# Optimization experiments

Measured on AMD Instinct MI355X. Metric: run time of the kernel, lower is better.

Reference implementation:

```python
import jax, jax.numpy as jnp
import numpy as np

D = 128
N1, N2, N3, N4 = 100000, 200000, 300000, 400000


def setup_inputs() -> dict:
    key = jax.random.key(0)
    cnt = [0]

    def nrm(shape, scale=0.05):
        cnt[0] += 1
        return jax.random.normal(jax.random.fold_in(key, cnt[0]), shape, dtype=jnp.float32) * scale

    def rint(shape, hi):
        cnt[0] += 1
        return jax.random.randint(jax.random.fold_in(key, cnt[0]), shape, 0, hi)

    inp = {}
    inp["h"] = nrm((N1, D), 1.0)
    inp["idx2"] = rint((N2, 2), N1)
    inp["idx3"] = rint((N3, 3), N1)
    inp["idx4"] = rint((N4, 4), N1)
    # sequential_%L MLPs: Linear(L*D -> D) + relu, Linear(D->D)+relu, Linear(D->D)+relu
    for L in (1, 2, 3, 4):
        din = D * L
        inp["s%d_W0" % L] = nrm((din, D))
        inp["s%d_b0" % L] = nrm((D,))
        inp["s%d_W1" % L] = nrm((D, D))
        inp["s%d_b1" % L] = nrm((D,))
        inp["s%d_W2" % L] = nrm((D, D))
        inp["s%d_b2" % L] = nrm((D,))
    # per-feature output heads Linear(D -> 1)
    for f in ("sigma", "epsilon", "q"):
        inp["h1_%s_W" % f] = nrm((D, 1))
        inp["h1_%s_b" % f] = nrm((1,))
    for L in (2, 3, 4):
        for f in ("k", "eq"):
            inp["h%d_%s_W" % (L, f)] = nrm((D, 1))
            inp["h%d_%s_b" % (L, f)] = nrm((1,))
    return inp


def _mlp(x, W0, b0, W1, b1, W2, b2):
    x = jax.nn.relu(x @ W0 + b0)
    x = jax.nn.relu(x @ W1 + b1)
    return jax.nn.relu(x @ W2 + b2)


def _level(h, idx, p):
    # copy_u + mean with exactly one n1 neighbor per relationship slot == gather
    g = jnp.take(h, idx, axis=0)              # [N, K, D]
    N, K, Dd = g.shape
    xf = g.reshape(N, K * Dd)                 # concat h0..h_{K-1}
    xb = g[:, ::-1, :].reshape(N, K * Dd)     # concat reversed
    return _mlp(xf, *p) + _mlp(xb, *p)        # pool = torch.add


def reference(h, idx2, idx3, idx4,
              s1_W0, s1_b0, s1_W1, s1_b1, s1_W2, s1_b2,
              s2_W0, s2_b0, s2_W1, s2_b1, s2_W2, s2_b2,
              s3_W0, s3_b0, s3_W1, s3_b1, s3_W2, s3_b2,
              s4_W0, s4_b0, s4_W1, s4_b1, s4_W2, s4_b2,
              h1_sigma_W, h1_sigma_b, h1_epsilon_W, h1_epsilon_b, h1_q_W, h1_q_b,
              h2_k_W, h2_k_b, h2_eq_W, h2_eq_b,
              h3_k_W, h3_k_b, h3_eq_W, h3_eq_b,
              h4_k_W, h4_k_b, h4_eq_W, h4_eq_b):
    y1 = _mlp(h, s1_W0, s1_b0, s1_W1, s1_b1, s1_W2, s1_b2)
    sigma = y1 @ h1_sigma_W + h1_sigma_b
    epsilon = y1 @ h1_epsilon_W + h1_epsilon_b
    q = y1 @ h1_q_W + h1_q_b
    y2 = _level(h, idx2, (s2_W0, s2_b0, s2_W1, s2_b1, s2_W2, s2_b2))
    k2 = y2 @ h2_k_W + h2_k_b
    eq2 = y2 @ h2_eq_W + h2_eq_b
    y3 = _level(h, idx3, (s3_W0, s3_b0, s3_W1, s3_b1, s3_W2, s3_b2))
    k3 = y3 @ h3_k_W + h3_k_b
    eq3 = y3 @ h3_eq_W + h3_eq_b
    y4 = _level(h, idx4, (s4_W0, s4_b0, s4_W1, s4_b1, s4_W2, s4_b2))
    k4 = y4 @ h4_k_W + h4_k_b
    eq4 = y4 @ h4_eq_W + h4_eq_b
    return (sigma, epsilon, q, k2, eq2, k3, eq3, k4, eq4)
```

## Files before the change

### kernel.cpp

```cpp
#include <hip/hip_runtime.h>

typedef __attribute__((ext_vector_type(8))) _Float16 half8;
typedef __attribute__((ext_vector_type(4))) float f32x4;

#define N1_ 100000
#define N2_ 200000
#define N3_ 300000
#define N4_ 400000

typedef __attribute__((address_space(1))) const void gconst_t;
typedef __attribute__((address_space(3))) void lds_t;

__device__ __forceinline__ unsigned short f2h_bits(float x) {
  union { _Float16 h; unsigned short u; } cv;
  cv.h = (_Float16)x;
  return cv.u;
}

__device__ __forceinline__ f32x4 mfma16(half8 a, half8 b, f32x4 c) {
  return __builtin_amdgcn_mfma_f32_16x16x32_f16(a, b, c, 0, 0, 0);
}

__global__ void cvt_h_kernel(const float* __restrict__ h,
                             unsigned short* __restrict__ hf, int n4) {
  int i = blockIdx.x * blockDim.x + threadIdx.x;
  if (i >= n4) return;
  float4 v = reinterpret_cast<const float4*>(h)[i];
  ushort4 o;
  o.x = f2h_bits(v.x); o.y = f2h_bits(v.y);
  o.z = f2h_bits(v.z); o.w = f2h_bits(v.w);
  reinterpret_cast<ushort4*>(hf)[i] = o;
}

struct PackInfo {
  const float* W[12];
  int kt_base[13];
  int out_off[12];
};

__global__ void pack_w_kernel(PackInfo info, unsigned short* __restrict__ pw) {
  int b = blockIdx.x;
  int lane = threadIdx.x;
  int m = 0;
  while (m < 11 && b >= info.kt_base[m + 1]) ++m;
  int kt = b - info.kt_base[m];
  const float* W = info.W[m];
  int lr = lane & 15, kb = lane >> 4;
  unsigned short* outp = pw + info.out_off[m] + (size_t)kt * 4096 + lane * 8;
  #pragma unroll
  for (int nt = 0; nt < 8; ++nt) {
    #pragma unroll
    for (int j = 0; j < 8; ++j) {
      int krow = kt * 32 + kb * 8 + j;
      int col = nt * 16 + lr;
      outp[nt * 512 + j] = f2h_bits(W[(size_t)krow * 128 + col]);
    }
  }
}

template <int K, int NHEAD>
__global__ __launch_bounds__(256, 3) void level_kernel(
    const unsigned short* __restrict__ hf,
    const int* __restrict__ idx,
    const unsigned short* __restrict__ pw,
    const float* __restrict__ b0, const float* __restrict__ b1,
    const float* __restrict__ b2,
    const float* __restrict__ hw0, const float* __restrict__ hb0,
    float* __restrict__ out0,
    const float* __restrict__ hw1, const float* __restrict__ hb1,
    float* __restrict__ out1,
    const float* __restrict__ hw2, const float* __restrict__ hb2,
    float* __restrict__ out2,
    int N) {
  constexpr int NDIR = (K > 1) ? 2 : 1;
  constexpr int KT0 = 4 * K;

  __shared__ __align__(16) unsigned short bstage[2][4096];
  __shared__ __align__(16) unsigned short act[4][NDIR][2048];

  const int lane = threadIdx.x & 63;
  const int wid = threadIdx.x >> 6;
  const int lrow = lane & 15;
  const int kb = lane >> 4;

  int tile = blockIdx.x * 4 + wid;
  const int maxtile = N / 16 - 1;
  const bool writer = (tile <= maxtile);
  if (!writer) tile = maxtile;
  const int row = tile * 16 + lrow;

  int src[K];
  #pragma unroll
  for (int s = 0; s < K; ++s) src[s] = (K == 1) ? row : idx[(size_t)row * K + s];

  auto stage = [&](int buf, const unsigned short* slab) {
    #pragma unroll
    for (int c = 0; c < 2; ++c) {
      const unsigned short* g = slab + (wid * 2 + c) * 512 + lane * 8;
      unsigned short* l = &bstage[buf][(wid * 2 + c) * 512];
      __builtin_amdgcn_global_load_lds((gconst_t*)g, (lds_t*)l, 16, 0, 0);
    }
  };

  int cur = 0;
  auto run_layer = [&](const unsigned short* w, int nkt, auto&& getAf,
                       auto&& getAb, f32x4* accF, f32x4* accB) {
    stage(cur, w);
    __syncthreads();
    for (int kt = 0; kt < nkt; ++kt) {
      if (kt + 1 < nkt) stage(cur ^ 1, w + (size_t)(kt + 1) * 4096);
      half8 af = getAf(kt);
      half8 ab;
      if constexpr (NDIR == 2) ab = getAb(kt);
      #pragma unroll
      for (int nt = 0; nt < 8; ++nt) {
        half8 bq = *reinterpret_cast<const half8*>(&bstage[cur][nt * 512 + lane * 8]);
        accF[nt] = mfma16(af, bq, accF[nt]);
        if constexpr (NDIR == 2) accB[nt] = mfma16(ab, bq, accB[nt]);
      }
      __syncthreads();
      cur ^= 1;
    }
  };

  auto A0f = [&](int kt) {
    int seg = kt >> 2, sub = kt & 3;
    return *reinterpret_cast<const half8*>(hf + (size_t)src[seg] * 128 + sub * 32 + kb * 8);
  };
  auto A0b = [&](int kt) {
    int seg = K - 1 - (kt >> 2), sub = kt & 3;
    return *reinterpret_cast<const half8*>(hf + (size_t)src[seg] * 128 + sub * 32 + kb * 8);
  };
  auto actRead = [&](int dir, int kt) -> half8 {
    unsigned off = (unsigned)(lrow * 256 + (kt * 32 + kb * 8) * 2) ^ ((unsigned)(lrow & 7) << 4);
    return *reinterpret_cast<const half8*>(
        reinterpret_cast<const unsigned char*>(&act[wid][dir][0]) + off);
  };
  auto actA0 = [&](int kt) { return actRead(0, kt); };
  auto actA1 = [&](int kt) { return actRead(NDIR == 2 ? 1 : 0, kt); };

  auto store_act = [&](const f32x4* acc, const float* bias, int dir) {
    unsigned char* base = reinterpret_cast<unsigned char*>(&act[wid][dir][0]);
    #pragma unroll
    for (int nt = 0; nt < 8; ++nt) {
      float bv = bias[nt * 16 + lrow];
      #pragma unroll
      for (int r = 0; r < 4; ++r) {
        float v = fmaxf(acc[nt][r] + bv, 0.f);
        int trow = 4 * kb + r;
        unsigned off = (unsigned)(trow * 256 + (nt * 16 + lrow) * 2) ^ ((unsigned)(trow & 7) << 4);
        *reinterpret_cast<unsigned short*>(base + off) = f2h_bits(v);
      }
    }
  };

  f32x4 aF[8], aB[8];
  auto zero_acc = [&](f32x4* a) {
    #pragma unroll
    for (int nt = 0; nt < 8; ++nt) a[nt] = f32x4{0.f, 0.f, 0.f, 0.f};
  };

  zero_acc(aF); zero_acc(aB);
  run_layer(pw, KT0, A0f, A0b, aF, aB);
  store_act(aF, b0, 0);
  if constexpr (NDIR == 2) store_act(aB, b0, 1);

  zero_acc(aF); zero_acc(aB);
  run_layer(pw + (size_t)KT0 * 4096, 4, actA0, actA1, aF, aB);
  store_act(aF, b1, 0);
  if constexpr (NDIR == 2) store_act(aB, b1, 1);

  zero_acc(aF); zero_acc(aB);
  run_layer(pw + (size_t)KT0 * 4096 + 16384, 4, actA0, actA1, aF, aB);

  f32x4 y[8];
  #pragma unroll
  for (int nt = 0; nt < 8; ++nt) {
    float bv = b2[nt * 16 + lrow];
    #pragma unroll
    for (int r = 0; r < 4; ++r) {
      float v = fmaxf(aF[nt][r] + bv, 0.f);
      if constexpr (NDIR == 2) v += fmaxf(aB[nt][r] + bv, 0.f);
      y[nt][r] = v;
    }
  }

  const float* hws[3] = {hw0, hw1, hw2};
  const float* hbs[3] = {hb0, hb1, hb2};
  float* outs[3] = {out0, out1, out2};
  #pragma unroll
  for (int hd = 0; hd < NHEAD; ++hd) {
    float p[4] = {0.f, 0.f, 0.f, 0.f};
    #pragma unroll
    for (int nt = 0; nt < 8; ++nt) {
      float w = hws[hd][nt * 16 + lrow];
      #pragma unroll
      for (int r = 0; r < 4; ++r) p[r] += y[nt][r] * w;
    }
    #pragma unroll
    for (int m = 1; m < 16; m <<= 1) {
      #pragma unroll
      for (int r = 0; r < 4; ++r) p[r] += __shfl_xor(p[r], m, 64);
    }
    if (writer && lrow < 4) {
      float pv = (lrow == 0) ? p[0] : (lrow == 1) ? p[1] : (lrow == 2) ? p[2] : p[3];
      outs[hd][tile * 16 + 4 * kb + lrow] = pv + hbs[hd][0];
    }
  }
}

extern "C" void kernel_launch(void* const* d_in, const int* in_sizes, int n_in,
                              void* d_out, int out_size, void* d_ws, size_t ws_size,
                              hipStream_t stream) {
  (void)in_sizes; (void)n_in; (void)out_size;

  const float* h = (const float*)d_in[0];
  const int* idx2 = (const int*)d_in[1];
  const int* idx3 = (const int*)d_in[2];
  const int* idx4 = (const int*)d_in[3];

  const float* sW[4][3];
  const float* sb[4][3];
  for (int L = 0; L < 4; ++L)
    for (int j = 0; j < 3; ++j) {
      sW[L][j] = (const float*)d_in[4 + L * 6 + j * 2];
      sb[L][j] = (const float*)d_in[4 + L * 6 + j * 2 + 1];
    }
  const float* hW[9];
  const float* hB[9];
  for (int i = 0; i < 9; ++i) {
    hW[i] = (const float*)d_in[28 + i * 2];
    hB[i] = (const float*)d_in[28 + i * 2 + 1];
  }

  size_t need = ((size_t)N1_ * 128 + 294912) * 2;
  if (ws_size < need) return;
  unsigned short* hf = (unsigned short*)d_ws;
  unsigned short* pw = hf + (size_t)N1_ * 128;

  cvt_h_kernel<<<(N1_ * 128 / 4 + 255) / 256, 256, 0, stream>>>(h, hf, N1_ * 128 / 4);

  PackInfo pi;
  const int din[12] = {128, 128, 128, 256, 128, 128, 384, 128, 128, 512, 128, 128};
  int ktb = 0, ooff = 0;
  for (int m = 0; m < 12; ++m) {
    pi.W[m] = sW[m / 3][m % 3];
    pi.kt_base[m] = ktb;
    pi.out_off[m] = ooff;
    ktb += din[m] / 32;
    ooff += din[m] * 128;
  }
  pi.kt_base[12] = ktb;
  pack_w_kernel<<<ktb, 64, 0, stream>>>(pi, pw);

  float* out = (float*)d_out;
  float* o_sigma = out;
  float* o_eps = out + N1_;
  float* o_q = out + 2 * N1_;
  float* o_k2 = out + 3 * N1_;
  float* o_eq2 = o_k2 + N2_;
  float* o_k3 = o_eq2 + N2_;
  float* o_eq3 = o_k3 + N3_;
  float* o_k4 = o_eq3 + N3_;
  float* o_eq4 = o_k4 + N4_;

  level_kernel<1, 3><<<(N1_ / 16 + 3) / 4, 256, 0, stream>>>(
      hf, nullptr, pw + pi.out_off[0], sb[0][0], sb[0][1], sb[0][2],
      hW[0], hB[0], o_sigma, hW[1], hB[1], o_eps, hW[2], hB[2], o_q, N1_);
  level_kernel<2, 2><<<(N2_ / 16 + 3) / 4, 256, 0, stream>>>(
      hf, idx2, pw + pi.out_off[3], sb[1][0], sb[1][1], sb[1][2],
      hW[3], hB[3], o_k2, hW[4], hB[4], o_eq2, nullptr, nullptr, nullptr, N2_);
  level_kernel<3, 2><<<(N3_ / 16 + 3) / 4, 256, 0, stream>>>(
      hf, idx3, pw + pi.out_off[6], sb[2][0], sb[2][1], sb[2][2],
      hW[5], hB[5], o_k3, hW[6], hB[6], o_eq3, nullptr, nullptr, nullptr, N3_);
  level_kernel<4, 2><<<(N4_ / 16 + 3) / 4, 256, 0, stream>>>(
      hf, idx4, pw + pi.out_off[9], sb[3][0], sb[3][1], sb[3][2],
      hW[7], hB[7], o_k4, hW[8], hB[8], o_eq4, nullptr, nullptr, nullptr, N4_);
}
```

Baseline: 506.5 us.

## Fuse MLP layers into one triple-buffered pipelined loop with gather prefetch

Replaces the per-layer double-buffered weight staging with a single loop over all k-steps of the three layers. It uses a three-slot LDS ring that stages two steps ahead, and prefetches the gathered activation rows two steps ahead in registers. It waits on explicit vmcnt counts instead of a full sync, and raises wave priority around the MFMA block. The goal is to hide global gather and weight-load latency and remove pipeline drains between layers. In exchange it uses more LDS and registers, and lowers the launch-bounds occupancy hint from 3 to 2 blocks.

Result: slower. 668.0 us (+31.9%).

```diff
diff --git a/kernel.cpp b/kernel.cpp
--- a/kernel.cpp
+++ b/kernel.cpp
@@ -59,7 +59,7 @@
 }
 
 template <int K, int NHEAD>
-__global__ __launch_bounds__(256, 3) void level_kernel(
+__global__ __launch_bounds__(256, 2) void level_kernel(
     const unsigned short* __restrict__ hf,
     const int* __restrict__ idx,
     const unsigned short* __restrict__ pw,
@@ -74,8 +74,9 @@
     int N) {
   constexpr int NDIR = (K > 1) ? 2 : 1;
   constexpr int KT0 = 4 * K;
-
-  __shared__ __align__(16) unsigned short bstage[2][4096];
+  constexpr int NS = KT0 + 8;
+
+  __shared__ __align__(16) unsigned short bstage[3][4096];
   __shared__ __align__(16) unsigned short act[4][NDIR][2048];
 
   const int lane = threadIdx.x & 63;
@@ -93,51 +94,25 @@
   #pragma unroll
   for (int s = 0; s < K; ++s) src[s] = (K == 1) ? row : idx[(size_t)row * K + s];
 
-  auto stage = [&](int buf, const unsigned short* slab) {
-    #pragma unroll
-    for (int c = 0; c < 2; ++c) {
-      const unsigned short* g = slab + (wid * 2 + c) * 512 + lane * 8;
-      unsigned short* l = &bstage[buf][(wid * 2 + c) * 512];
-      __builtin_amdgcn_global_load_lds((gconst_t*)g, (lds_t*)l, 16, 0, 0);
-    }
-  };
-
-  int cur = 0;
-  auto run_layer = [&](const unsigned short* w, int nkt, auto&& getAf,
-                       auto&& getAb, f32x4* accF, f32x4* accB) {
-    stage(cur, w);
-    __syncthreads();
-    for (int kt = 0; kt < nkt; ++kt) {
-      if (kt + 1 < nkt) stage(cur ^ 1, w + (size_t)(kt + 1) * 4096);
-      half8 af = getAf(kt);
-      half8 ab;
-      if constexpr (NDIR == 2) ab = getAb(kt);
-      #pragma unroll
-      for (int nt = 0; nt < 8; ++nt) {
-        half8 bq = *reinterpret_cast<const half8*>(&bstage[cur][nt * 512 + lane * 8]);
-        accF[nt] = mfma16(af, bq, accF[nt]);
-        if constexpr (NDIR == 2) accB[nt] = mfma16(ab, bq, accB[nt]);
-      }
-      __syncthreads();
-      cur ^= 1;
-    }
-  };
-
-  auto A0f = [&](int kt) {
+  auto stage_s = [&](int buf, int s) {
+    const unsigned short* g = pw + (size_t)s * 4096 + (wid * 2) * 512 + lane * 8;
+    unsigned short* l = &bstage[buf][(wid * 2) * 512];
+    __builtin_amdgcn_global_load_lds((gconst_t*)g, (lds_t*)l, 16, 0, 0);
+    __builtin_amdgcn_global_load_lds((gconst_t*)(g + 512), (lds_t*)(l + 512), 16, 0, 0);
+  };
+
+  auto gload = [&](int kt, half8& f, half8& b) {
     int seg = kt >> 2, sub = kt & 3;
-    return *reinterpret_cast<const half8*>(hf + (size_t)src[seg] * 128 + sub * 32 + kb * 8);
-  };
-  auto A0b = [&](int kt) {
-    int seg = K - 1 - (kt >> 2), sub = kt & 3;
-    return *reinterpret_cast<const half8*>(hf + (size_t)src[seg] * 128 + sub * 32 + kb * 8);
-  };
+    f = *reinterpret_cast<const half8*>(hf + (size_t)src[seg] * 128 + sub * 32 + kb * 8);
+    if constexpr (NDIR == 2)
+      b = *reinterpret_cast<const half8*>(hf + (size_t)src[K - 1 - seg] * 128 + sub * 32 + kb * 8);
+  };
+
   auto actRead = [&](int dir, int kt) -> half8 {
     unsigned off = (unsigned)(lrow * 256 + (kt * 32 + kb * 8) * 2) ^ ((unsigned)(lrow & 7) << 4);
     return *reinterpret_cast<const half8*>(
         reinterpret_cast<const unsigned char*>(&act[wid][dir][0]) + off);
   };
-  auto actA0 = [&](int kt) { return actRead(0, kt); };
-  auto actA1 = [&](int kt) { return actRead(NDIR == 2 ? 1 : 0, kt); };
 
   auto store_act = [&](const f32x4* acc, const float* bias, int dir) {
     unsigned char* base = reinterpret_cast<unsigned char*>(&act[wid][dir][0]);
@@ -155,23 +130,71 @@
   };
 
   f32x4 aF[8], aB[8];
-  auto zero_acc = [&](f32x4* a) {
-    #pragma unroll
-    for (int nt = 0; nt < 8; ++nt) a[nt] = f32x4{0.f, 0.f, 0.f, 0.f};
-  };
-
-  zero_acc(aF); zero_acc(aB);
-  run_layer(pw, KT0, A0f, A0b, aF, aB);
-  store_act(aF, b0, 0);
-  if constexpr (NDIR == 2) store_act(aB, b0, 1);
-
-  zero_acc(aF); zero_acc(aB);
-  run_layer(pw + (size_t)KT0 * 4096, 4, actA0, actA1, aF, aB);
-  store_act(aF, b1, 0);
-  if constexpr (NDIR == 2) store_act(aB, b1, 1);
-
-  zero_acc(aF); zero_acc(aB);
-  run_layer(pw + (size_t)KT0 * 4096 + 16384, 4, actA0, actA1, aF, aB);
+  auto zero_acc = [&]() {
+    #pragma unroll
+    for (int nt = 0; nt < 8; ++nt) {
+      aF[nt] = f32x4{0.f, 0.f, 0.f, 0.f};
+      if constexpr (NDIR == 2) aB[nt] = f32x4{0.f, 0.f, 0.f, 0.f};
+    }
+  };
+  zero_acc();
+
+  half8 gf0{}, gb0{}, gf1{}, gb1{};
+  stage_s(0, 0);
+  stage_s(1, 1);
+  gload(0, gf0, gb0);
+  gload(1, gf1, gb1);
+
+  int rdBuf = 0, stBuf = 2;
+
+  for (int s = 0; s < NS; ++s) {
+    __builtin_amdgcn_sched_barrier(0);
+    const int kwait = (s + 1 < NS ? 2 : 0) + (s + 1 < KT0 ? NDIR : 0);
+    if (kwait == 4)      asm volatile("s_waitcnt vmcnt(4)" ::: "memory");
+    else if (kwait == 3) asm volatile("s_waitcnt vmcnt(3)" ::: "memory");
+    else if (kwait == 2) asm volatile("s_waitcnt vmcnt(2)" ::: "memory");
+    else                 asm volatile("s_waitcnt vmcnt(0)" ::: "memory");
+    __builtin_amdgcn_s_barrier();
+    __builtin_amdgcn_sched_barrier(0);
+
+    if (s + 2 < NS) stage_s(stBuf, s + 2);
+    half8 nf{}, nb{};
+    if (s + 2 < KT0) gload(s + 2, nf, nb);
+
+    half8 af, ab;
+    if (s < KT0) {
+      af = gf0;
+      if constexpr (NDIR == 2) ab = gb0;
+    } else {
+      int kt = (s - KT0) & 3;
+      af = actRead(0, kt);
+      if constexpr (NDIR == 2) ab = actRead(1, kt);
+    }
+
+    __builtin_amdgcn_s_setprio(1);
+    #pragma unroll
+    for (int nt = 0; nt < 8; ++nt) {
+      half8 bq = *reinterpret_cast<const half8*>(&bstage[rdBuf][nt * 512 + lane * 8]);
+      aF[nt] = mfma16(af, bq, aF[nt]);
+      if constexpr (NDIR == 2) aB[nt] = mfma16(ab, bq, aB[nt]);
+    }
+    __builtin_amdgcn_s_setprio(0);
+
+    gf0 = gf1; gf1 = nf;
+    if constexpr (NDIR == 2) { gb0 = gb1; gb1 = nb; }
+    rdBuf = (rdBuf == 2) ? 0 : rdBuf + 1;
+    stBuf = (stBuf == 2) ? 0 : stBuf + 1;
+
+    if (s == KT0 - 1) {
+      store_act(aF, b0, 0);
+      if constexpr (NDIR == 2) store_act(aB, b0, 1);
+      zero_acc();
+    } else if (s == KT0 + 3) {
+      store_act(aF, b1, 0);
+      if constexpr (NDIR == 2) store_act(aB, b1, 1);
+      zero_acc();
+    }
+  }
 
   f32x4 y[8];
   #pragma unroll
```

## Process two row tiles per wave and prefetch gathered A fragments

Applied to the files above, without the earlier changes.

Each wavefront now handles two 16-row tiles instead of one, so every staged weight slab in LDS feeds twice as many MFMAs. The first layer also prefetches the gathered activation fragments for the next k-step from global memory while the current step computes. Grid size is halved and launch bounds drop to two blocks per SIMD to make room for the doubled accumulator register footprint. The cost is higher register and LDS use per block, which lowers occupancy.

New measurement: 522.4 us. +3.1%, slower.

```diff
diff --git a/kernel.cpp b/kernel.cpp
--- a/kernel.cpp
+++ b/kernel.cpp
@@ -59,7 +59,7 @@
 }
 
 template <int K, int NHEAD>
-__global__ __launch_bounds__(256, 3) void level_kernel(
+__global__ __launch_bounds__(256, 2) void level_kernel(
     const unsigned short* __restrict__ hf,
     const int* __restrict__ idx,
     const unsigned short* __restrict__ pw,
@@ -76,135 +76,186 @@
   constexpr int KT0 = 4 * K;
 
   __shared__ __align__(16) unsigned short bstage[2][4096];
-  __shared__ __align__(16) unsigned short act[4][NDIR][2048];
+  __shared__ __align__(16) unsigned short act[4][NDIR][2][2048];
 
   const int lane = threadIdx.x & 63;
   const int wid = threadIdx.x >> 6;
   const int lrow = lane & 15;
   const int kb = lane >> 4;
 
-  int tile = blockIdx.x * 4 + wid;
+  const int wtile = (blockIdx.x * 4 + wid) * 2;
   const int maxtile = N / 16 - 1;
-  const bool writer = (tile <= maxtile);
-  if (!writer) tile = maxtile;
-  const int row = tile * 16 + lrow;
-
-  int src[K];
-  #pragma unroll
-  for (int s = 0; s < K; ++s) src[s] = (K == 1) ? row : idx[(size_t)row * K + s];
+  int tile[2];
+  bool wr[2];
+  #pragma unroll
+  for (int t = 0; t < 2; ++t) {
+    wr[t] = (wtile + t <= maxtile);
+    tile[t] = wr[t] ? (wtile + t) : maxtile;
+  }
+
+  int src[2][K];
+  #pragma unroll
+  for (int t = 0; t < 2; ++t)
+    #pragma unroll
+    for (int s = 0; s < K; ++s)
+      src[t][s] = (K == 1) ? (tile[t] * 16 + lrow)
+                           : idx[(size_t)(tile[t] * 16 + lrow) * K + s];
 
   auto stage = [&](int buf, const unsigned short* slab) {
-    #pragma unroll
-    for (int c = 0; c < 2; ++c) {
-      const unsigned short* g = slab + (wid * 2 + c) * 512 + lane * 8;
-      unsigned short* l = &bstage[buf][(wid * 2 + c) * 512];
-      __builtin_amdgcn_global_load_lds((gconst_t*)g, (lds_t*)l, 16, 0, 0);
+    const unsigned short* g = slab + (wid * 2) * 512 + lane * 8;
+    unsigned short* l = &bstage[buf][(wid * 2) * 512];
+    __builtin_amdgcn_global_load_lds((gconst_t*)g, (lds_t*)l, 16, 0, 0);
+    __builtin_amdgcn_global_load_lds((gconst_t*)(g + 512), (lds_t*)(l + 512), 16, 0, 0);
+  };
+
+  auto gload = [&](int kt, half8 (*f)[NDIR]) {
+    int seg = kt >> 2, sub = kt & 3;
+    #pragma unroll
+    for (int t = 0; t < 2; ++t) {
+      f[t][0] = *reinterpret_cast<const half8*>(
+          hf + (size_t)src[t][seg] * 128 + sub * 32 + kb * 8);
+      if constexpr (NDIR == 2)
+        f[t][1] = *reinterpret_cast<const half8*>(
+            hf + (size_t)src[t][K - 1 - seg] * 128 + sub * 32 + kb * 8);
+    }
+  };
+
+  auto actA = [&](int t, int d, int kt) -> half8 {
+    unsigned off = (unsigned)(lrow * 256 + (kt * 32 + kb * 8) * 2) ^
+                   ((unsigned)(lrow & 7) << 4);
+    return *reinterpret_cast<const half8*>(
+        reinterpret_cast<const unsigned char*>(&act[wid][d][t][0]) + off);
+  };
+
+  f32x4 acc[2][NDIR][8];
+  auto zero_acc = [&]() {
+    #pragma unroll
+    for (int t = 0; t < 2; ++t)
+      #pragma unroll
+      for (int d = 0; d < NDIR; ++d)
+        #pragma unroll
+        for (int nt = 0; nt < 8; ++nt) acc[t][d][nt] = f32x4{0.f, 0.f, 0.f, 0.f};
+  };
+
+  auto store_act = [&](int t, int d, const float* bias) {
+    unsigned char* base = reinterpret_cast<unsigned char*>(&act[wid][d][t][0]);
+    #pragma unroll
+    for (int nt = 0; nt < 8; ++nt) {
+      float bv = bias[nt * 16 + lrow];
+      #pragma unroll
+      for (int r = 0; r < 4; ++r) {
+        float v = fmaxf(acc[t][d][nt][r] + bv, 0.f);
+        int trow = 4 * kb + r;
+        unsigned off = (unsigned)(trow * 256 + (nt * 16 + lrow) * 2) ^
+                       ((unsigned)(trow & 7) << 4);
+        *reinterpret_cast<unsigned short*>(base + off) = f2h_bits(v);
+      }
     }
   };
 
   int cur = 0;
-  auto run_layer = [&](const unsigned short* w, int nkt, auto&& getAf,
-                       auto&& getAb, f32x4* accF, f32x4* accB) {
+
+  zero_acc();
+  half8 aCur[2][NDIR], aNxt[2][NDIR];
+  stage(cur, pw);
+  gload(0, aCur);
+  __syncthreads();
+  for (int kt = 0; kt < KT0; ++kt) {
+    if (kt + 1 < KT0) {
+      stage(cur ^ 1, pw + (size_t)(kt + 1) * 4096);
+      gload(kt + 1, aNxt);
+    }
+    #pragma unroll
+    for (int nt = 0; nt < 8; ++nt) {
+      half8 bq = *reinterpret_cast<const half8*>(&bstage[cur][nt * 512 + lane * 8]);
+      #pragma unroll
+      for (int t = 0; t < 2; ++t)
+        #pragma unroll
+        for (int d = 0; d < NDIR; ++d)
+          acc[t][d][nt] = mfma16(aCur[t][d], bq, acc[t][d][nt]);
+    }
+    __syncthreads();
+    cur ^= 1;
+    #pragma unroll
+    for (int t = 0; t < 2; ++t)
+      #pragma unroll
+      for (int d = 0; d < NDIR; ++d) aCur[t][d] = aNxt[t][d];
+  }
+  #pragma unroll
+  for (int t = 0; t < 2; ++t)
+    #pragma unroll
+    for (int d = 0; d < NDIR; ++d) store_act(t, d, b0);
+
+  const unsigned short* wptr[2] = {pw + (size_t)KT0 * 4096,
+                                   pw + (size_t)KT0 * 4096 + 16384};
+  #pragma unroll 1
+  for (int layer = 1; layer <= 2; ++layer) {
+    const unsigned short* w = wptr[layer - 1];
+    zero_acc();
     stage(cur, w);
     __syncthreads();
-    for (int kt = 0; kt < nkt; ++kt) {
-      if (kt + 1 < nkt) stage(cur ^ 1, w + (size_t)(kt + 1) * 4096);
-      half8 af = getAf(kt);
-      half8 ab;
-      if constexpr (NDIR == 2) ab = getAb(kt);
+    for (int kt = 0; kt < 4; ++kt) {
+      if (kt + 1 < 4) stage(cur ^ 1, w + (size_t)(kt + 1) * 4096);
+      half8 a[2][NDIR];
+      #pragma unroll
+      for (int t = 0; t < 2; ++t)
+        #pragma unroll
+        for (int d = 0; d < NDIR; ++d) a[t][d] = actA(t, d, kt);
       #pragma unroll
       for (int nt = 0; nt < 8; ++nt) {
         half8 bq = *reinterpret_cast<const half8*>(&bstage[cur][nt * 512 + lane * 8]);
-        accF[nt] = mfma16(af, bq, accF[nt]);
-        if constexpr (NDIR == 2) accB[nt] = mfma16(ab, bq, accB[nt]);
+        #pragma unroll
+        for (int t = 0; t < 2; ++t)
+          #pragma unroll
+          for (int d = 0; d < NDIR; ++d)
+            acc[t][d][nt] = mfma16(a[t][d], bq, acc[t][d][nt]);
       }
       __syncthreads();
       cur ^= 1;
     }
-  };
-
-  auto A0f = [&](int kt) {
-    int seg = kt >> 2, sub = kt & 3;
-    return *reinterpret_cast<const half8*>(hf + (size_t)src[seg] * 128 + sub * 32 + kb * 8);
-  };
-  auto A0b = [&](int kt) {
-    int seg = K - 1 - (kt >> 2), sub = kt & 3;
-    return *reinterpret_cast<const half8*>(hf + (size_t)src[seg] * 128 + sub * 32 + kb * 8);
-  };
-  auto actRead = [&](int dir, int kt) -> half8 {
-    unsigned off = (unsigned)(lrow * 256 + (kt * 32 + kb * 8) * 2) ^ ((unsigned)(lrow & 7) << 4);
-    return *reinterpret_cast<const half8*>(
-        reinterpret_cast<const unsigned char*>(&act[wid][dir][0]) + off);
-  };
-  auto actA0 = [&](int kt) { return actRead(0, kt); };
-  auto actA1 = [&](int kt) { return actRead(NDIR == 2 ? 1 : 0, kt); };
-
-  auto store_act = [&](const f32x4* acc, const float* bias, int dir) {
-    unsigned char* base = reinterpret_cast<unsigned char*>(&act[wid][dir][0]);
-    #pragma unroll
-    for (int nt = 0; nt < 8; ++nt) {
-      float bv = bias[nt * 16 + lrow];
-      #pragma unroll
-      for (int r = 0; r < 4; ++r) {
-        float v = fmaxf(acc[nt][r] + bv, 0.f);
-        int trow = 4 * kb + r;
-        unsigned off = (unsigned)(trow * 256 + (nt * 16 + lrow) * 2) ^ ((unsigned)(trow & 7) << 4);
-        *reinterpret_cast<unsigned short*>(base + off) = f2h_bits(v);
-      }
-    }
-  };
-
-  f32x4 aF[8], aB[8];
-  auto zero_acc = [&](f32x4* a) {
-    #pragma unroll
-    for (int nt = 0; nt < 8; ++nt) a[nt] = f32x4{0.f, 0.f, 0.f, 0.f};
-  };
-
-  zero_acc(aF); zero_acc(aB);
-  run_layer(pw, KT0, A0f, A0b, aF, aB);
-  store_act(aF, b0, 0);
-  if constexpr (NDIR == 2) store_act(aB, b0, 1);
-
-  zero_acc(aF); zero_acc(aB);
-  run_layer(pw + (size_t)KT0 * 4096, 4, actA0, actA1, aF, aB);
-  store_act(aF, b1, 0);
-  if constexpr (NDIR == 2) store_act(aB, b1, 1);
-
-  zero_acc(aF); zero_acc(aB);
-  run_layer(pw + (size_t)KT0 * 4096 + 16384, 4, actA0, actA1, aF, aB);
-
-  f32x4 y[8];
-  #pragma unroll
-  for (int nt = 0; nt < 8; ++nt) {
-    float bv = b2[nt * 16 + lrow];
-    #pragma unroll
-    for (int r = 0; r < 4; ++r) {
-      float v = fmaxf(aF[nt][r] + bv, 0.f);
-      if constexpr (NDIR == 2) v += fmaxf(aB[nt][r] + bv, 0.f);
-      y[nt][r] = v;
+    if (layer == 1) {
+      #pragma unroll
+      for (int t = 0; t < 2; ++t)
+        #pragma unroll
+        for (int d = 0; d < NDIR; ++d) store_act(t, d, b1);
     }
   }
 
   const float* hws[3] = {hw0, hw1, hw2};
   const float* hbs[3] = {hb0, hb1, hb2};
   float* outs[3] = {out0, out1, out2};
-  #pragma unroll
-  for (int hd = 0; hd < NHEAD; ++hd) {
-    float p[4] = {0.f, 0.f, 0.f, 0.f};
+
+  #pragma unroll
+  for (int t = 0; t < 2; ++t) {
+    f32x4 y[8];
     #pragma unroll
     for (int nt = 0; nt < 8; ++nt) {
-      float w = hws[hd][nt * 16 + lrow];
-      #pragma unroll
-      for (int r = 0; r < 4; ++r) p[r] += y[nt][r] * w;
-    }
-    #pragma unroll
-    for (int m = 1; m < 16; m <<= 1) {
-      #pragma unroll
-      for (int r = 0; r < 4; ++r) p[r] += __shfl_xor(p[r], m, 64);
-    }
-    if (writer && lrow < 4) {
-      float pv = (lrow == 0) ? p[0] : (lrow == 1) ? p[1] : (lrow == 2) ? p[2] : p[3];
-      outs[hd][tile * 16 + 4 * kb + lrow] = pv + hbs[hd][0];
+      float bv = b2[nt * 16 + lrow];
+      #pragma unroll
+      for (int r = 0; r < 4; ++r) {
+        float v = fmaxf(acc[t][0][nt][r] + bv, 0.f);
+        if constexpr (NDIR == 2) v += fmaxf(acc[t][1][nt][r] + bv, 0.f);
+        y[nt][r] = v;
+      }
+    }
+    #pragma unroll
+    for (int hd = 0; hd < NHEAD; ++hd) {
+      float p[4] = {0.f, 0.f, 0.f, 0.f};
+      #pragma unroll
+      for (int nt = 0; nt < 8; ++nt) {
+        float w = hws[hd][nt * 16 + lrow];
+        #pragma unroll
+        for (int r = 0; r < 4; ++r) p[r] += y[nt][r] * w;
+      }
+      #pragma unroll
+      for (int m = 1; m < 16; m <<= 1) {
+        #pragma unroll
+        for (int r = 0; r < 4; ++r) p[r] += __shfl_xor(p[r], m, 64);
+      }
+      if (wr[t] && lrow < 4) {
+        float pv = (lrow == 0) ? p[0] : (lrow == 1) ? p[1] : (lrow == 2) ? p[2] : p[3];
+        outs[hd][tile[t] * 16 + 4 * kb + lrow] = pv + hbs[hd][0];
+      }
     }
   }
 }
@@ -264,16 +315,16 @@
   float* o_k4 = o_eq3 + N3_;
   float* o_eq4 = o_k4 + N4_;
 
-  level_kernel<1, 3><<<(N1_ / 16 + 3) / 4, 256, 0, stream>>>(
+  level_kernel<1, 3><<<(N1_ / 16 + 7) / 8, 256, 0, stream>>>(
       hf, nullptr, pw + pi.out_off[0], sb[0][0], sb[0][1], sb[0][2],
       hW[0], hB[0], o_sigma, hW[1], hB[1], o_eps, hW[2], hB[2], o_q, N1_);
-  level_kernel<2, 2><<<(N2_ / 16 + 3) / 4, 256, 0, stream>>>(
+  level_kernel<2, 2><<<(N2_ / 16 + 7) / 8, 256, 0, stream>>>(
       hf, idx2, pw + pi.out_off[3], sb[1][0], sb[1][1], sb[1][2],
       hW[3], hB[3], o_k2, hW[4], hB[4], o_eq2, nullptr, nullptr, nullptr, N2_);
-  level_kernel<3, 2><<<(N3_ / 16 + 3) / 4, 256, 0, stream>>>(
+  level_kernel<3, 2><<<(N3_ / 16 + 7) / 8, 256, 0, stream>>>(
       hf, idx3, pw + pi.out_off[6], sb[2][0], sb[2][1], sb[2][2],
       hW[5], hB[5], o_k3, hW[6], hB[6], o_eq3, nullptr, nullptr, nullptr, N3_);
-  level_kernel<4, 2><<<(N4_ / 16 + 3) / 4, 256, 0, stream>>>(
+  level_kernel<4, 2><<<(N4_ / 16 + 7) / 8, 256, 0, stream>>>(
       hf, idx4, pw + pi.out_off[9], sb[3][0], sb[3][1], sb[3][2],
       hW[7], hB[7], o_k4, hW[8], hB[8], o_eq4, nullptr, nullptr, nullptr, N4_);
 }
```
